# Optimization experiments

Measured on AMD Instinct MI355X. Metric: run time of the kernel, lower is better.

Reference implementation:

```python
import jax, jax.numpy as jnp
import numpy as np

B, T, C = 2, 2048, 2048
NH = 16            # query heads
NKV = NH // 2      # kv heads (GQA)
HD = C // NH       # head dim = 128
N_REP = NH // NKV  # 2


def setup_inputs() -> dict:
    key = jax.random.key(0)
    k1, k2, k3 = jax.random.split(key, 3)
    x = jax.random.normal(k1, (B, T, C), jnp.float32)
    w_attn = jax.random.normal(k2, (C, (NH + 2 * NKV) * HD), jnp.float32) * 0.02
    w_proj = jax.random.normal(k3, (C, C), jnp.float32) * 0.02
    t = jnp.arange(T, dtype=jnp.float32)
    inv_freq = 1.0 / (10000.0 ** (jnp.arange(0, HD, 2, dtype=jnp.float32) / HD))
    freqs = t[:, None] * inv_freq[None, :]  # [T, HD//2]
    return {"x": x, "w_attn": w_attn, "w_proj": w_proj,
            "freqs_cos": jnp.cos(freqs), "freqs_sin": jnp.sin(freqs)}


def _rope(v, cos, sin):
    # v: [B, T, H, HD]; complex multiply on (even, odd) pairs
    vr = v.reshape(*v.shape[:-1], HD // 2, 2)
    x0, x1 = vr[..., 0], vr[..., 1]
    c = cos[None, :, None, :]
    s = sin[None, :, None, :]
    o0 = x0 * c - x1 * s
    o1 = x0 * s + x1 * c
    return jnp.stack([o0, o1], axis=-1).reshape(v.shape)


def reference(x, w_attn, w_proj, freqs_cos, freqs_sin):
    qkv = x @ w_attn  # [B, T, (NH+2*NKV)*HD]
    q, k, v = jnp.split(qkv, [NH * HD, (NH + NKV) * HD], axis=-1)
    q = q.reshape(B, T, NH, HD)
    k = k.reshape(B, T, NKV, HD)
    v = v.reshape(B, T, NKV, HD)
    q = _rope(q, freqs_cos, freqs_sin)
    k = _rope(k, freqs_cos, freqs_sin)
    # GQA: group query heads over kv heads instead of repeating k/v
    q = q.transpose(0, 2, 1, 3).reshape(B, NKV, N_REP, T, HD)  # [B, G, R, T, HD]
    k = k.transpose(0, 2, 1, 3)  # [B, G, T, HD]
    v = v.transpose(0, 2, 1, 3)  # [B, G, T, HD]
    scale = jnp.float32(1.0 / np.sqrt(HD))
    scores = jnp.einsum('bgrqd,bgkd->bgrqk', q, k) * scale
    causal = jnp.tril(jnp.ones((T, T), dtype=bool))
    scores = jnp.where(causal, scores, jnp.float32(-1e30))
    p = jax.nn.softmax(scores, axis=-1)
    y = jnp.einsum('bgrqk,bgkd->bgrqd', p, v)  # [B, G, R, T, HD]
    y = y.reshape(B, NH, T, HD).transpose(0, 2, 1, 3).reshape(B, T, C)
    return y @ w_proj
```

## Files before the change

### kernel.cpp

```cpp
#include <hip/hip_runtime.h>
#include <hip/hip_bf16.h>
#include <stdint.h>
#include <stddef.h>

typedef unsigned short u16;
using bf16x8 = __attribute__((ext_vector_type(8))) short;
using f32x4  = __attribute__((ext_vector_type(4))) float;
using f32x16 = __attribute__((ext_vector_type(16))) float;

#define DEVFN static __device__ __forceinline__

DEVFN u16 f2b(float f){ __hip_bfloat16 h = __float2bfloat16(f); return *reinterpret_cast<u16*>(&h); }
DEVFN float b2f(u16 u){ __hip_bfloat16 h; *reinterpret_cast<u16*>(&h) = u; return __bfloat162float(h); }
DEVFN uint32_t pk2(float a, float b){
  uint32_t r; asm("v_cvt_pk_bf16_f32 %0, %1, %2" : "=v"(r) : "v"(a), "v"(b)); return r;
}
DEVFN float ex2(float x){ float r; asm("v_exp_f32 %0, %1" : "=v"(r) : "v"(x)); return r; }

DEVFN void gload_lds16(const void* g, void* l){
  __builtin_amdgcn_global_load_lds(
      (const __attribute__((address_space(1))) void*)g,
      (__attribute__((address_space(3))) void*)l, 16, 0, 0);
}

__global__ void detect_k(const uint32_t* __restrict__ fc_raw, uint32_t* __restrict__ flag){
  if (threadIdx.x == 0 && blockIdx.x == 0)
    flag[0] = (fc_raw[0] == 0x3F800000u) ? 1u : 0u;
}

__global__ __launch_bounds__(256) void cvtf_k(const void* __restrict__ in, float* __restrict__ out,
                                              int n, const uint32_t* __restrict__ flag){
  const int i = blockIdx.x*256 + threadIdx.x;
  if (i >= n) return;
  if (flag[0]) out[i] = ((const float*)in)[i];
  else         out[i] = b2f(((const u16*)in)[i]);
}

__global__ __launch_bounds__(256) void cvtx_k(const void* __restrict__ in, u16* __restrict__ out,
                                              int n8, const uint32_t* __restrict__ flag){
  const int i = blockIdx.x*256 + threadIdx.x;
  if (i >= n8) return;
  __align__(16) u16 e[8];
  if (flag[0]){
    const float* f = (const float*)in + (size_t)i*8;
    float4 a = *(const float4*)f, b = *(const float4*)(f+4);
    e[0]=f2b(a.x); e[1]=f2b(a.y); e[2]=f2b(a.z); e[3]=f2b(a.w);
    e[4]=f2b(b.x); e[5]=f2b(b.y); e[6]=f2b(b.z); e[7]=f2b(b.w);
  } else {
    *(uint4*)e = *((const uint4*)in + i);
  }
  *(uint4*)(out + (size_t)i*8) = *(const uint4*)e;
}

__global__ __launch_bounds__(512) void wtrans_k(const void* __restrict__ in, u16* __restrict__ out,
                                                int C, int R, const uint32_t* __restrict__ flag){
  __shared__ __align__(16) u16 tile[64][72];
  const int r0 = blockIdx.y*64, c0 = blockIdx.x*64;
  const int t = threadIdx.x, r = t>>3, cs = (t&7)*8;
  __align__(16) u16 e[8];
  if (flag[0]){
    const float* f = (const float*)in + (size_t)(r0+r)*C + c0 + cs;
    float4 a = *(const float4*)f, b = *(const float4*)(f+4);
    e[0]=f2b(a.x); e[1]=f2b(a.y); e[2]=f2b(a.z); e[3]=f2b(a.w);
    e[4]=f2b(b.x); e[5]=f2b(b.y); e[6]=f2b(b.z); e[7]=f2b(b.w);
  } else {
    *(uint4*)e = *(const uint4*)((const u16*)in + (size_t)(r0+r)*C + c0 + cs);
  }
#pragma unroll
  for (int j=0;j<8;j++) tile[cs+j][r] = e[j];
  __syncthreads();
  uint4 o = *(const uint4*)&tile[r][cs];
  *(uint4*)(out + (size_t)(c0+r)*R + r0 + cs) = o;
}

__global__ __launch_bounds__(512) void vtrans_k(const u16* __restrict__ qkv, u16* __restrict__ vT){
  __shared__ __align__(16) u16 tile[64][72];
  const int z = blockIdx.z, b = z>>3, g = z&7;
  const u16* in = qkv + (size_t)(b*2048)*4096 + 3072 + g*128;
  u16* out = vT + (size_t)z*128*2048;
  const int r0 = blockIdx.y*64, c0 = blockIdx.x*64;
  const int t = threadIdx.x, r = t>>3, cs = (t&7)*8;
  uint4 v = *(const uint4*)(in + (size_t)(r0+r)*4096 + c0 + cs);
  const u16* e = (const u16*)&v;
#pragma unroll
  for (int j=0;j<8;j++) tile[cs+j][r] = e[j];
  __syncthreads();
  uint4 o = *(const uint4*)&tile[r][cs];
  *(uint4*)(out + (size_t)(c0+r)*2048 + r0 + cs) = o;
}

__global__ __launch_bounds__(256) void rope_k(u16* qkv, const float* __restrict__ fc,
                                              const float* __restrict__ fs){
  const int idx = blockIdx.x*256 + threadIdx.x;
  const int row = idx / 1536;
  const int p   = idx % 1536;
  const int col0 = p*2;
  const int t = row & 2047;
  const int i = p & 63;
  uint32_t* ptr = (uint32_t*)(qkv + (size_t)row*4096 + col0);
  uint32_t u = *ptr;
  float x0 = b2f((u16)(u & 0xffff));
  float x1 = b2f((u16)(u >> 16));
  float c = fc[t*64+i], s = fs[t*64+i];
  float o0 = x0*c - x1*s;
  float o1 = x0*s + x1*c;
  if (col0 < 2048){
    const float S2 = 0.08838834764831845f * 1.4426950408889634f;
    o0 *= S2; o1 *= S2;
  }
  *ptr = (uint32_t)f2b(o0) | ((uint32_t)f2b(o1) << 16);
}

__global__ __launch_bounds__(256) void gemm_bt(const u16* __restrict__ A, const u16* __restrict__ Bt,
                                               void* __restrict__ Cv, int M, int N, int K,
                                               const uint32_t* __restrict__ flag, int fin){
  __shared__ __align__(16) u16 Al[2][128*32];
  __shared__ __align__(16) u16 Bl[2][128*32];
  const int nwg_x = N>>7;
  int wg = blockIdx.x;
  {
    const int nwg = gridDim.x;
    const int cpx = nwg >> 3;
    wg = (wg & 7)*cpx + (wg >> 3);
  }
  const int tm = (wg / nwg_x)*128, tn = (wg % nwg_x)*128;
  const int tid = threadIdx.x, w = tid>>6, l = tid&63, lr = l&15, lg = l>>4;
  const int wr = w>>1, wc = w&1;

  f32x4 acc[4][4] = {};

  auto stage = [&](int buf, int kk){
#pragma unroll
    for (int issue=0; issue<2; ++issue){
      const int c = issue*256 + w*64 + l;
      const int r = c>>2, sl = c&3;
      const int gch = sl ^ (r&3);
      gload_lds16(A  + (size_t)(tm + r)*K + kk + gch*8, &Al[buf][(issue*256 + w*64)*8]);
      gload_lds16(Bt + (size_t)(tn + r)*K + kk + gch*8, &Bl[buf][(issue*256 + w*64)*8]);
    }
  };

  stage(0, 0);
  __syncthreads();
  const int nk = K>>5;
  for (int kt=0; kt<nk; ++kt){
    if (kt+1 < nk) stage((kt+1)&1, (kt+1)*32);
    const u16* Ab = Al[kt&1];
    const u16* Bb = Bl[kt&1];
    bf16x8 a[4], b[4];
#pragma unroll
    for (int mi=0;mi<4;mi++){
      const int rr = wr*64 + mi*16 + lr;
      a[mi] = *(const bf16x8*)&Ab[rr*32 + ((lg ^ (rr&3))*8)];
    }
#pragma unroll
    for (int ni=0;ni<4;ni++){
      const int rr = wc*64 + ni*16 + lr;
      b[ni] = *(const bf16x8*)&Bb[rr*32 + ((lg ^ (rr&3))*8)];
    }
#pragma unroll
    for (int mi=0;mi<4;mi++)
#pragma unroll
      for (int ni=0;ni<4;ni++)
        acc[mi][ni] = __builtin_amdgcn_mfma_f32_16x16x32_bf16(a[mi], b[ni], acc[mi][ni], 0,0,0);
    __syncthreads();
  }
  const bool of32 = fin && (flag[0] != 0);
#pragma unroll
  for (int mi=0;mi<4;mi++)
#pragma unroll
    for (int ni=0;ni<4;ni++)
#pragma unroll
      for (int reg=0;reg<4;reg++){
        const int row = tm + wr*64 + mi*16 + lg*4 + reg;
        const int col = tn + wc*64 + ni*16 + lr;
        const size_t idx = (size_t)row*N + col;
        const float v = acc[mi][ni][reg];
        if (of32) ((float*)Cv)[idx] = v;
        else      ((u16*)Cv)[idx]   = f2b(v);
      }
}

__global__ __launch_bounds__(512, 1) void attn_k(const u16* __restrict__ qkv,
                                                 const u16* __restrict__ vT,
                                                 u16* __restrict__ y){
  __shared__ __align__(16) u16 KV[2][2][16384];
  const int i0 = blockIdx.x;
  const int g  = i0 & 7;
  const int r1 = i0 >> 3;
  const int hl = r1 & 1;
  const int vq = (r1 >> 1) & 7;
  const int b  = r1 >> 4;
  const int h  = g*2 + hl;

  const int tid = threadIdx.x;
  const int w = tid >> 6, l = tid & 63;
  const int grp = w >> 2, wq = w & 3;
  const int lq = l & 31;
  const int hi = l >> 5;

  const u16* kg = qkv + (size_t)(b*2048)*4096 + 2048 + g*128;
  const u16* vg = vT  + (size_t)(b*8+g)*128*2048;

  const int rk = tid >> 2, cb = tid & 3;
  uint4 kpre[4], vpre[4];
  auto loadT = [&](int kvbase){
#pragma unroll
    for (int j=0;j<4;j++){
      const int ch = cb + j*4;
      kpre[j] = *(const uint4*)(kg + (size_t)(kvbase + rk)*4096 + ch*8);
      vpre[j] = *(const uint4*)(vg + (size_t)rk*2048 + kvbase + ch*8);
    }
  };
  auto writeT = [&](int buf){
    u16* Kd = &KV[buf][rk>>6][0];
    const int rl = rk & 63;
#pragma unroll
    for (int j=0;j<4;j++){
      const int ch = cb + j*4;
      *(uint4*)&Kd[rl*128 + ((ch ^ (rl&15))*8)] = kpre[j];
    }
#pragma unroll
    for (int j=0;j<4;j++){
      const int ch = cb + j*4;
      u16* Vd = &KV[buf][ch>>3][8192];
      *(uint4*)&Vd[rk*64 + (((ch&7) ^ (rk&7))*8)] = vpre[j];
    }
  };

  int qt = vq;
  const int nA = vq + 1;
  bf16x8 qf[8];
  f32x16 yacc[4];
  float mrow, lsum;

  auto loadQ = [&]{
    const size_t qrow = (size_t)(b*2048 + qt*128 + wq*32 + lq);
    const u16* qp = qkv + qrow*4096 + h*128 + hi*8;
#pragma unroll
    for (int ds=0; ds<8; ++ds) qf[ds] = *(const bf16x8*)(qp + ds*16);
  };
  auto resetAcc = [&]{
#pragma unroll
    for (int dt=0; dt<4; ++dt)
#pragma unroll
      for (int r=0; r<16; ++r) yacc[dt][r] = 0.f;
    mrow = -1e30f; lsum = 0.f;
  };

  auto mergePhase = [&](u16* Mb){
    float* Mm = (float*)Mb; float* Ml = Mm + 128;
    u16* MOs = Mb + 512 + wq*4096;
    __syncthreads();
    if (grp == 1){
      if (l < 32){ Mm[wq*32 + l] = mrow; Ml[wq*32 + l] = lsum; }
#pragma unroll
      for (int dt=0; dt<4; ++dt)
#pragma unroll
        for (int rq=0; rq<4; ++rq){
          const int d0 = dt*32 + rq*8 + hi*4;
          uint32_t lo = pk2(yacc[dt][rq*4+0], yacc[dt][rq*4+1]);
          uint32_t hi2= pk2(yacc[dt][rq*4+2], yacc[dt][rq*4+3]);
          const int idx = (lq*128 + d0) ^ ((lq&7)<<3);
          *(uint2*)&MOs[idx] = make_uint2(lo, hi2);
        }
    }
    __syncthreads();
    if (grp == 0){
      const float mo = Mm[wq*32 + lq], lo_ = Ml[wq*32 + lq];
      const float ms = fmaxf(mrow, mo);
      const float ce = ex2(mrow - ms), co = ex2(mo - ms);
      const float inv = 1.f / (lsum*ce + lo_*co);
#pragma unroll
      for (int dt=0; dt<4; ++dt)
#pragma unroll
        for (int rq=0; rq<4; ++rq){
          const int d0 = dt*32 + rq*8 + hi*4;
          const int idx = (lq*128 + d0) ^ ((lq&7)<<3);
          uint2 pr = *(const uint2*)&MOs[idx];
          const float yo0 = b2f((u16)(pr.x & 0xffff)), yo1 = b2f((u16)(pr.x >> 16));
          const float yo2 = b2f((u16)(pr.y & 0xffff)), yo3 = b2f((u16)(pr.y >> 16));
          uint32_t lo = pk2((yacc[dt][rq*4+0]*ce + yo0*co)*inv, (yacc[dt][rq*4+1]*ce + yo1*co)*inv);
          uint32_t hi2= pk2((yacc[dt][rq*4+2]*ce + yo2*co)*inv, (yacc[dt][rq*4+3]*ce + yo3*co)*inv);
          *(uint2*)&MOs[idx] = make_uint2(lo, hi2);
        }
    }
    __syncthreads();
    const int qb2 = b*2048 + qt*128 + wq*32;
#pragma unroll
    for (int p=0; p<2; ++p){
      const int row = grp*16 + p*8 + (l>>3);
      const int gc = l & 7;
      const int idx0 = (row*128 + gc*16) ^ ((row&7)<<3);
      const int idx1 = (row*128 + gc*16 + 8) ^ ((row&7)<<3);
      uint4 v0 = *(const uint4*)&MOs[idx0];
      uint4 v1 = *(const uint4*)&MOs[idx1];
      u16* yp = y + (size_t)(qb2 + row)*2048 + h*128 + gc*16;
      *(uint4*)yp = v0;
      *(uint4*)(yp + 8) = v1;
    }
    __syncthreads();
  };

  loadT(0); writeT(0); __syncthreads();
  loadQ(); resetAcc();

  for (int s=0; s<17; ++s){
    if (s == nA){
      mergePhase(&KV[(nA&1)^1][0][0]);
      qt = 15 - vq;
      loadQ(); resetAcc();
    }
    const int sj = (s < nA) ? s : s - nA;
    const int kvbase = sj*128;
    if (s+1 < 17){
      const int s2 = s+1;
      const int sj2 = (s2 < nA) ? s2 : s2 - nA;
      loadT(sj2*128);
    }
    const u16* Kb = &KV[s&1][grp][0];
    const u16* Vb = Kb + 8192;
    const int tilebase = kvbase + grp*64;
    const int qmin = qt*128 + wq*32;
    const int qrow = qmin + lq;

    if (tilebase <= qmin + 31){
      f32x16 sc[2];
#pragma unroll
      for (int t=0;t<2;t++)
#pragma unroll
        for (int r=0;r<16;r++) sc[t][r] = 0.f;
      __builtin_amdgcn_s_setprio(1);
#pragma unroll
      for (int t=0; t<2; ++t){
        const int r = t*32 + lq;
        const int rsw = r & 15;
#pragma unroll
        for (int ds=0; ds<8; ++ds){
          const bf16x8 kf = *(const bf16x8*)&Kb[r*128 + (((2*ds+hi) ^ rsw)*8)];
          sc[t] = __builtin_amdgcn_mfma_f32_32x32x16_bf16(kf, qf[ds], sc[t], 0,0,0);
        }
      }
      __builtin_amdgcn_s_setprio(0);

      if (tilebase + 63 > qmin){
#pragma unroll
        for (int t=0;t<2;t++)
#pragma unroll
          for (int r=0;r<16;r++){
            const int kp = tilebase + t*32 + (r&3) + 8*(r>>2) + 4*hi;
            if (kp > qrow) sc[t][r] = -1e30f;
          }
      }

      float mx[16];
#pragma unroll
      for (int r=0;r<16;r++) mx[r] = fmaxf(sc[0][r], sc[1][r]);
#pragma unroll
      for (int off=8; off>0; off>>=1)
#pragma unroll
        for (int r=0;r<8;r++)
          if (r < off) mx[r] = fmaxf(mx[r], mx[r+off]);
      float pmax = fmaxf(mx[0], __shfl_xor(mx[0], 32));

      if (!__all(pmax <= mrow + 8.f)){
        const float mnew = fmaxf(mrow, pmax);
        const float corr = ex2(mrow - mnew);
        mrow = mnew; lsum *= corr;
#pragma unroll
        for (int dt=0;dt<4;dt++)
#pragma unroll
          for (int r=0;r<16;r++) yacc[dt][r] *= corr;
      }

#pragma unroll
      for (int t=0;t<2;t++)
#pragma unroll
        for (int r=0;r<16;r++) sc[t][r] = ex2(sc[t][r] - mrow);
      float sm[16];
#pragma unroll
      for (int r=0;r<16;r++) sm[r] = sc[0][r] + sc[1][r];
#pragma unroll
      for (int off=8; off>0; off>>=1)
#pragma unroll
        for (int r=0;r<8;r++)
          if (r < off) sm[r] += sm[r+off];
      lsum += sm[0] + __shfl_xor(sm[0], 32);

      __align__(16) uint32_t pw[4][4];
#pragma unroll
      for (int t=0;t<2;t++)
#pragma unroll
        for (int half=0; half<2; ++half){
          const int q8 = half*8;
          const uint32_t X0 = pk2(sc[t][q8+0], sc[t][q8+1]);
          const uint32_t X1 = pk2(sc[t][q8+2], sc[t][q8+3]);
          const uint32_t X2 = pk2(sc[t][q8+4], sc[t][q8+5]);
          const uint32_t X3 = pk2(sc[t][q8+6], sc[t][q8+7]);
          const uint32_t pX0 = (uint32_t)__shfl_xor((int)X0, 32);
          const uint32_t pX1 = (uint32_t)__shfl_xor((int)X1, 32);
          const uint32_t pX2 = (uint32_t)__shfl_xor((int)X2, 32);
          const uint32_t pX3 = (uint32_t)__shfl_xor((int)X3, 32);
          const int ks = t*2 + half;
          pw[ks][0] = hi ? pX2 : X0;
          pw[ks][1] = hi ? pX3 : X1;
          pw[ks][2] = hi ? X2 : pX0;
          pw[ks][3] = hi ? X3 : pX1;
        }

      __builtin_amdgcn_s_setprio(1);
#pragma unroll
      for (int dt=0; dt<4; ++dt){
        const int d = dt*32 + lq;
        const int dsw = d & 7;
#pragma unroll
        for (int ks=0; ks<4; ++ks){
          const bf16x8 vf = *(const bf16x8*)&Vb[d*64 + (((2*ks+hi) ^ dsw)*8)];
          yacc[dt] = __builtin_amdgcn_mfma_f32_32x32x16_bf16(vf, *(const bf16x8*)&pw[ks][0], yacc[dt], 0,0,0);
        }
      }
      __builtin_amdgcn_s_setprio(0);
    }

    if (s+1 < 17) writeT((s&1)^1);
    __syncthreads();
  }
  mergePhase(&KV[0][0][0]);
}

extern "C" void kernel_launch(void* const* d_in, const int* in_sizes, int n_in,
                              void* d_out, int out_size, void* d_ws, size_t ws_size,
                              hipStream_t stream){
  char* ws = (char*)d_ws;
  const size_t MB = 1048576;
  uint32_t* flag = (uint32_t*)(ws);
  float* fcF = (float*)(ws + 1*MB);
  float* fsF = (float*)(ws + 1*MB + 524288);
  u16* xb   = (u16*)(ws + 2*MB);
  u16* waT  = (u16*)(ws + 18*MB);
  u16* wpT  = (u16*)(ws + 34*MB);
  u16* qkvb = (u16*)(ws + 42*MB);
  u16* vTb  = (u16*)(ws + 74*MB);
  u16* yb   = xb;

  detect_k<<<1, 64, 0, stream>>>((const uint32_t*)d_in[3], flag);
  cvtf_k  <<<512, 256, 0, stream>>>(d_in[3], fcF, 131072, flag);
  cvtf_k  <<<512, 256, 0, stream>>>(d_in[4], fsF, 131072, flag);
  cvtx_k  <<<4096, 256, 0, stream>>>(d_in[0], xb, 1048576, flag);
  wtrans_k<<<dim3(64,32,1), 512, 0, stream>>>(d_in[1], waT, 4096, 2048, flag);
  wtrans_k<<<dim3(32,32,1), 512, 0, stream>>>(d_in[2], wpT, 2048, 2048, flag);
  gemm_bt <<<dim3(1024,1,1), 256, 0, stream>>>(xb, waT, qkvb, 4096, 4096, 2048, flag, 0);
  rope_k  <<<dim3(24576,1,1), 256, 0, stream>>>(qkvb, fcF, fsF);
  vtrans_k<<<dim3(2,32,16), 512, 0, stream>>>(qkvb, vTb);
  attn_k  <<<dim3(256,1,1), 512, 0, stream>>>(qkvb, vTb, yb);
  gemm_bt <<<dim3(512,1,1), 256, 0, stream>>>(yb, wpT, d_out, 4096, 2048, 2048, flag, 1);
}
```

Before: 295.8 us.

## Rewrite GEMM with 256x128 tiles, 8 waves, and triple-buffered async LDS pipeline

Replaces the 128x128 double-buffered GEMM with a 512-thread kernel computing 256x128 tiles. Global-to-LDS loads run two stages ahead in three buffers, and partial vmcnt waits with raw s_barrier replace __syncthreads. The LDS swizzle also mixes in row>>2 to cut bank conflicts. The goal is better latency hiding and B-tile reuse, at the cost of more LDS per block and fewer workgroups.

```diff
diff --git a/kernel.cpp b/kernel.cpp
--- a/kernel.cpp
+++ b/kernel.cpp
@@ -111,60 +111,71 @@
   *ptr = (uint32_t)f2b(o0) | ((uint32_t)f2b(o1) << 16);
 }
 
-__global__ __launch_bounds__(256) void gemm_bt(const u16* __restrict__ A, const u16* __restrict__ Bt,
-                                               void* __restrict__ Cv, int M, int N, int K,
-                                               const uint32_t* __restrict__ flag, int fin){
-  __shared__ __align__(16) u16 Al[2][128*32];
-  __shared__ __align__(16) u16 Bl[2][128*32];
+__global__ __launch_bounds__(512) void gemm_p(const u16* __restrict__ A, const u16* __restrict__ Bt,
+                                              void* __restrict__ Cv, int M, int N, int K,
+                                              const uint32_t* __restrict__ flag, int fin){
+  __shared__ __align__(16) u16 L[3*12288];
   const int nwg_x = N>>7;
   int wg = blockIdx.x;
-  {
-    const int nwg = gridDim.x;
-    const int cpx = nwg >> 3;
-    wg = (wg & 7)*cpx + (wg >> 3);
-  }
-  const int tm = (wg / nwg_x)*128, tn = (wg % nwg_x)*128;
+  { const int cpx = (int)gridDim.x >> 3; wg = (wg&7)*cpx + (wg>>3); }
+  const int tm = (wg / nwg_x)*256, tn = (wg % nwg_x)*128;
   const int tid = threadIdx.x, w = tid>>6, l = tid&63, lr = l&15, lg = l>>4;
-  const int wr = w>>1, wc = w&1;
+  const int wm = w>>1, wn = w&1;
 
   f32x4 acc[4][4] = {};
 
-  auto stage = [&](int buf, int kk){
-#pragma unroll
-    for (int issue=0; issue<2; ++issue){
-      const int c = issue*256 + w*64 + l;
-      const int r = c>>2, sl = c&3;
-      const int gch = sl ^ (r&3);
-      gload_lds16(A  + (size_t)(tm + r)*K + kk + gch*8, &Al[buf][(issue*256 + w*64)*8]);
-      gload_lds16(Bt + (size_t)(tn + r)*K + kk + gch*8, &Bl[buf][(issue*256 + w*64)*8]);
-    }
-  };
-
-  stage(0, 0);
-  __syncthreads();
+  auto stage = [&](int kt, int buf){
+    const int kk = kt*32;
+    u16* Lb = &L[buf*12288];
+#pragma unroll
+    for (int j=0;j<2;j++){
+      const int s = j*512 + tid;
+      const int row = s>>2, c = s&3;
+      const int gch = c ^ ((row ^ (row>>2)) & 3);
+      gload_lds16(A + (size_t)(tm + row)*K + kk + gch*8, &Lb[(j*512 + w*64)*8]);
+    }
+    {
+      const int s = tid;
+      const int row = s>>2, c = s&3;
+      const int gch = c ^ ((row ^ (row>>2)) & 3);
+      gload_lds16(Bt + (size_t)(tn + row)*K + kk + gch*8, &Lb[8192 + (w*64)*8]);
+    }
+  };
+
   const int nk = K>>5;
+  stage(0,0); stage(1,1);
+  asm volatile("s_waitcnt vmcnt(3)" ::: "memory");
+  __builtin_amdgcn_s_barrier();
+  __builtin_amdgcn_sched_barrier(0);
+
   for (int kt=0; kt<nk; ++kt){
-    if (kt+1 < nk) stage((kt+1)&1, (kt+1)*32);
-    const u16* Ab = Al[kt&1];
-    const u16* Bb = Bl[kt&1];
+    const int buf = kt % 3;
+    if (kt+2 < nk) stage(kt+2, (kt+2) % 3);
+    const u16* Ab = &L[buf*12288];
+    const u16* Bb = Ab + 8192;
     bf16x8 a[4], b[4];
 #pragma unroll
     for (int mi=0;mi<4;mi++){
-      const int rr = wr*64 + mi*16 + lr;
-      a[mi] = *(const bf16x8*)&Ab[rr*32 + ((lg ^ (rr&3))*8)];
+      const int row = wm*64 + mi*16 + lr;
+      a[mi] = *(const bf16x8*)&Ab[row*32 + ((lg ^ ((row ^ (row>>2))&3))*8)];
     }
 #pragma unroll
     for (int ni=0;ni<4;ni++){
-      const int rr = wc*64 + ni*16 + lr;
-      b[ni] = *(const bf16x8*)&Bb[rr*32 + ((lg ^ (rr&3))*8)];
+      const int row = wn*64 + ni*16 + lr;
+      b[ni] = *(const bf16x8*)&Bb[row*32 + ((lg ^ ((row ^ (row>>2))&3))*8)];
     }
 #pragma unroll
     for (int mi=0;mi<4;mi++)
 #pragma unroll
       for (int ni=0;ni<4;ni++)
         acc[mi][ni] = __builtin_amdgcn_mfma_f32_16x16x32_bf16(a[mi], b[ni], acc[mi][ni], 0,0,0);
-    __syncthreads();
+    __builtin_amdgcn_sched_barrier(0);
+    if (kt+2 < nk) asm volatile("s_waitcnt vmcnt(3)" ::: "memory");
+    else           asm volatile("s_waitcnt vmcnt(0)" ::: "memory");
+    __builtin_amdgcn_s_barrier();
+    __builtin_amdgcn_sched_barrier(0);
   }
+
   const bool of32 = fin && (flag[0] != 0);
 #pragma unroll
   for (int mi=0;mi<4;mi++)
@@ -172,8 +183,8 @@
     for (int ni=0;ni<4;ni++)
 #pragma unroll
       for (int reg=0;reg<4;reg++){
-        const int row = tm + wr*64 + mi*16 + lg*4 + reg;
-        const int col = tn + wc*64 + ni*16 + lr;
+        const int row = tm + wm*64 + mi*16 + lg*4 + reg;
+        const int col = tn + wn*64 + ni*16 + lr;
         const size_t idx = (size_t)row*N + col;
         const float v = acc[mi][ni][reg];
         if (of32) ((float*)Cv)[idx] = v;
@@ -449,9 +460,9 @@
   cvtx_k  <<<4096, 256, 0, stream>>>(d_in[0], xb, 1048576, flag);
   wtrans_k<<<dim3(64,32,1), 512, 0, stream>>>(d_in[1], waT, 4096, 2048, flag);
   wtrans_k<<<dim3(32,32,1), 512, 0, stream>>>(d_in[2], wpT, 2048, 2048, flag);
-  gemm_bt <<<dim3(1024,1,1), 256, 0, stream>>>(xb, waT, qkvb, 4096, 4096, 2048, flag, 0);
+  gemm_p  <<<dim3(512,1,1), 512, 0, stream>>>(xb, waT, qkvb, 4096, 4096, 2048, flag, 0);
   rope_k  <<<dim3(24576,1,1), 256, 0, stream>>>(qkvb, fcF, fsF);
   vtrans_k<<<dim3(2,32,16), 512, 0, stream>>>(qkvb, vTb);
   attn_k  <<<dim3(256,1,1), 512, 0, stream>>>(qkvb, vTb, yb);
-  gemm_bt <<<dim3(512,1,1), 256, 0, stream>>>(yb, wpT, d_out, 4096, 2048, 2048, flag, 1);
-}
+  gemm_p  <<<dim3(256,1,1), 512, 0, stream>>>(yb, wpT, d_out, 4096, 2048, 2048, flag, 1);
+}
```

Result: faster. 271.4 us (-8.3%).
